# Kernel optimization log

Hardware: AMD Instinct MI355X
Metric: run time of the kernel (lower is better)

## Reference

```python
import jax, jax.numpy as jnp
import numpy as np
import math

N_HEAD = 16

def setup_inputs() -> dict:
    key = jax.random.key(0)
    ks = jax.random.split(key, 5)
    B, T, C = 4, 2048, 2048
    s = 1.0 / math.sqrt(C)
    return {
        "x": jax.random.normal(ks[0], (B, T, C), jnp.float32),
        "w_attn": jax.random.normal(ks[1], (C, 3 * C), jnp.float32) * s,
        "b_attn": jax.random.normal(ks[2], (3 * C,), jnp.float32) * 0.01,
        "w_proj": jax.random.normal(ks[3], (C, C), jnp.float32) * s,
        "b_proj": jax.random.normal(ks[4], (C,), jnp.float32) * 0.01,
    }

def reference(x, w_attn, b_attn, w_proj, b_proj):
    B, T, C = x.shape
    H = N_HEAD
    D = C // H
    # fused QKV projection: [B,T,3C] -> [3,B,H,T,D]
    qkv = (x @ w_attn + b_attn).reshape(B, T, 3, H, D).transpose(2, 0, 3, 1, 4)
    q, k, v = qkv[0], qkv[1], qkv[2]
    scale = 1.0 / math.sqrt(D)
    scores = jnp.einsum("bhqd,bhkd->bhqk", q, k) * scale  # [B,H,T,T]
    causal = jnp.tril(jnp.ones((T, T), dtype=bool))
    neg = jnp.finfo(scores.dtype).min
    scores = jnp.where(causal, scores, neg)
    attn = jax.nn.softmax(scores, axis=-1)
    y = jnp.einsum("bhqk,bhkd->bhqd", attn, v)  # [B,H,T,D]
    y = y.transpose(0, 2, 1, 3).reshape(B, T, C)
    return y @ w_proj + b_proj
```

## Files before the change

kernel.cpp:

```cpp
#include <hip/hip_runtime.h>
#include <hip/hip_bf16.h>
#include <stdint.h>

typedef unsigned short u16;
typedef __bf16 bf16x8 __attribute__((ext_vector_type(8)));
typedef unsigned short u16x8 __attribute__((ext_vector_type(8)));
typedef float f32x4 __attribute__((ext_vector_type(4)));

__device__ __forceinline__ float bf2f(u16 u){ union{float f; unsigned i;} v; v.i = ((unsigned)u)<<16; return v.f; }
__device__ __forceinline__ u16 f2bf(float f){ union{float f; unsigned i;} v; v.f=f; unsigned r = v.i + 0x7FFFu + ((v.i>>16)&1u); return (u16)(r>>16); }

__device__ __forceinline__ void async16(const void* g, void* l){
  __builtin_amdgcn_global_load_lds((const __attribute__((address_space(1))) void*)g,
                                   (__attribute__((address_space(3))) void*)l, 16, 0, 0);
}

__global__ __launch_bounds__(256) void cvt_f2b(const float* __restrict__ src, u16* __restrict__ dst, int n)
{
  int i = (blockIdx.x * 256 + threadIdx.x) * 4;
  if (i < n) {
    float4 v = *(const float4*)&src[i];
    ushort4 o;
    o.x = f2bf(v.x); o.y = f2bf(v.y); o.z = f2bf(v.z); o.w = f2bf(v.w);
    *(ushort4*)&dst[i] = o;
  }
}

__global__ __launch_bounds__(256) void transpose2d_f2b(const float* __restrict__ src, u16* __restrict__ dst,
                                                       int src_rows, int src_cols)
{
  __shared__ u16 tile[64][72];
  const int r0 = blockIdx.y << 6, c0 = blockIdx.x << 6;
  const int t = threadIdx.x;
  #pragma unroll
  for (int i=0;i<4;i++){
    int slot = t + (i<<8);
    int r = slot >> 4, cv = (slot & 15) << 2;
    float4 v = *(const float4*)&src[(size_t)(r0+r)*src_cols + c0 + cv];
    tile[r][cv+0] = f2bf(v.x); tile[r][cv+1] = f2bf(v.y);
    tile[r][cv+2] = f2bf(v.z); tile[r][cv+3] = f2bf(v.w);
  }
  __syncthreads();
  #pragma unroll
  for (int i=0;i<2;i++){
    int slot = t + (i<<8);
    int cr = slot >> 3, rv = (slot & 7) << 3;
    u16x8 v;
    #pragma unroll
    for (int e=0;e<8;e++) v[e] = tile[rv+e][cr];
    *(u16x8*)&dst[(size_t)(c0+cr)*src_rows + r0 + rv] = v;
  }
}

__global__ __launch_bounds__(256) void transpose_v(const u16* __restrict__ qkv, u16* __restrict__ vt)
{
  __shared__ u16 tile[64][72];
  const int bh = blockIdx.z;
  const int b = bh >> 4, h = bh & 15;
  const u16* src = qkv + (size_t)b*2048*6144 + 4096 + h*128;
  u16* dst = vt + (size_t)bh*128*2048;
  const int t0 = blockIdx.y << 6, d0 = blockIdx.x << 6;
  const int t = threadIdx.x;
  #pragma unroll
  for (int i=0;i<2;i++){
    int slot = t + (i<<8);
    int r = slot >> 3, cv = (slot & 7) << 3;
    *(u16x8*)&tile[r][cv] = *(const u16x8*)&src[(size_t)(t0+r)*6144 + d0 + cv];
  }
  __syncthreads();
  #pragma unroll
  for (int i=0;i<2;i++){
    int slot = t + (i<<8);
    int cr = slot >> 3, rv = (slot & 7) << 3;
    u16x8 v;
    #pragma unroll
    for (int e=0;e<8;e++) v[e] = tile[rv+e][cr];
    *(u16x8*)&dst[(size_t)(d0+cr)*2048 + t0 + rv] = v;
  }
}

template<int F32OUT>
__global__ __launch_bounds__(512, 2) void gemm8p(const u16* __restrict__ A, const u16* __restrict__ Bt,
                                                 const float* __restrict__ bias, void* __restrict__ Cv,
                                                 int M, int N, int K, int mtiles)
{
  __shared__ u16 lsA[2][2][256*32];
  __shared__ u16 lsB[2][2][256*32];
  const int tid = threadIdx.x;
  const int w = tid >> 6, lane = tid & 63;
  const int wm = w >> 2, wn = w & 3;
  const int lo = lane & 15, hi = lane >> 4;

  const int nwg = gridDim.x;
  const int bid = blockIdx.x;
  const int swz = (bid & 7) * (nwg >> 3) + (bid >> 3);
  const int mt = swz % mtiles, nt = swz / mtiles;
  const int m0 = mt << 8, n0 = nt << 8;
  const int NT = K >> 6, NI = NT >> 1;

  const int s0 = tid, s1 = tid + 512;
  const size_t off0 = (size_t)(s0>>2)*K + (size_t)((((s0&3) ^ ((s0>>3)&3))) << 3);
  const size_t off1 = (size_t)(s1>>2)*K + (size_t)((((s1&3) ^ ((s1>>3)&3))) << 3);
  const u16* Asrc = A + (size_t)m0*K;
  const u16* Bsrc = Bt + (size_t)n0*K;

  f32x4 acc[8][4];
  f32x4 z = {0.f,0.f,0.f,0.f};
  #pragma unroll
  for (int i=0;i<8;i++)
    #pragma unroll
    for (int j=0;j<4;j++) acc[i][j] = z;

  bf16x8 aE[4], aO[4], bX[4], bY[4];

#define SLOT(T, KH, AP, BP) do { \
    const u16* as_ = Asrc + (T)*64 + (KH)*32; \
    const u16* bs_ = Bsrc + (T)*64 + (KH)*32; \
    async16(as_ + off0, &(AP)[s0*8]); \
    async16(as_ + off1, &(AP)[s1*8]); \
    async16(bs_ + off0, &(BP)[s0*8]); \
    async16(bs_ + off1, &(BP)[s1*8]); \
  } while(0)

#define RDA(SET, BUF, KS, Q) do { \
    _Pragma("unroll") \
    for (int mf=0; mf<4; ++mf){ \
      int row_ = wm*128 + (Q)*64 + mf*16 + lo; \
      SET[mf] = *(const bf16x8*)&lsA[BUF][KS][row_*32 + ((hi ^ ((row_>>1) & 3)) << 3)]; \
    } } while(0)

#define RDB(SET, BUF, KS) do { \
    _Pragma("unroll") \
    for (int nf=0; nf<4; ++nf){ \
      int row_ = wn*64 + nf*16 + lo; \
      SET[nf] = *(const bf16x8*)&lsB[BUF][KS][row_*32 + ((hi ^ ((row_>>1) & 3)) << 3)]; \
    } } while(0)

#define MM(Q, AS, BS) do { \
    __builtin_amdgcn_s_setprio(1); \
    _Pragma("unroll") \
    for (int mf=0; mf<4; ++mf) \
      _Pragma("unroll") \
      for (int nf=0; nf<4; ++nf) \
        acc[(Q)*4+mf][nf] = __builtin_amdgcn_mfma_f32_16x16x32_bf16(AS[mf], BS[nf], acc[(Q)*4+mf][nf], 0,0,0); \
    __builtin_amdgcn_s_setprio(0); \
  } while(0)

#define LGK4 do { asm volatile("s_waitcnt lgkmcnt(4)" ::: "memory"); __builtin_amdgcn_sched_barrier(0); } while(0)
#define LGK8 do { asm volatile("s_waitcnt lgkmcnt(8)" ::: "memory"); __builtin_amdgcn_sched_barrier(0); } while(0)
#define LGK0 do { asm volatile("s_waitcnt lgkmcnt(0)" ::: "memory"); __builtin_amdgcn_sched_barrier(0); } while(0)
#define VM8 asm volatile("s_waitcnt vmcnt(8)" ::: "memory")
#define VM4 asm volatile("s_waitcnt vmcnt(4)" ::: "memory")
#define VM0 asm volatile("s_waitcnt vmcnt(0)" ::: "memory")
#define ENDP do { __builtin_amdgcn_s_barrier(); __builtin_amdgcn_sched_barrier(0); } while(0)

  SLOT(0, 0, lsA[0][0], lsB[0][0]);
  SLOT(0, 1, lsA[0][1], lsB[0][1]);
  SLOT(1, 0, lsA[1][0], lsB[1][0]);
  VM8;
  __builtin_amdgcn_s_barrier();
  __builtin_amdgcn_sched_barrier(0);
  RDA(aO, 0,0, 0); RDB(bX, 0,0);

  #pragma unroll 1
  for (int i = 0; i < NI-1; ++i){
    const int t0 = 2*i;
    RDA(aE, 0,0, 1); SLOT(t0+1,1, lsA[1][1], lsB[1][1]); LGK4; MM(0, aO, bX); VM8; ENDP;
    RDA(aO, 0,1, 0); RDB(bY, 0,1);                       LGK8; MM(1, aE, bX);      ENDP;
    RDA(aE, 0,1, 1); SLOT(t0+2,0, lsA[0][0], lsB[0][0]); LGK4; MM(0, aO, bY); VM8; ENDP;
    RDA(aO, 1,0, 0); RDB(bX, 1,0);                       LGK8; MM(1, aE, bY);      ENDP;
    RDA(aE, 1,0, 1); SLOT(t0+2,1, lsA[0][1], lsB[0][1]); LGK4; MM(0, aO, bX); VM8; ENDP;
    RDA(aO, 1,1, 0); RDB(bY, 1,1);                       LGK8; MM(1, aE, bX);      ENDP;
    RDA(aE, 1,1, 1); SLOT(t0+3,0, lsA[1][0], lsB[1][0]); LGK4; MM(0, aO, bY); VM8; ENDP;
    RDA(aO, 0,0, 0); RDB(bX, 0,0);                       LGK8; MM(1, aE, bY);      ENDP;
  }
  RDA(aE, 0,0, 1); SLOT(NT-1,1, lsA[1][1], lsB[1][1]);   LGK4; MM(0, aO, bX); VM8; ENDP;
  RDA(aO, 0,1, 0); RDB(bY, 0,1);                         LGK8; MM(1, aE, bX);      ENDP;
  RDA(aE, 0,1, 1);                                       LGK4; MM(0, aO, bY); VM4; ENDP;
  RDA(aO, 1,0, 0); RDB(bX, 1,0);                         LGK8; MM(1, aE, bY);      ENDP;
  RDA(aE, 1,0, 1);                                       LGK4; MM(0, aO, bX); VM0; ENDP;
  RDA(aO, 1,1, 0); RDB(bY, 1,1);                         LGK8; MM(1, aE, bX);      ENDP;
  RDA(aE, 1,1, 1);                                       LGK4; MM(0, aO, bY);      ENDP;
                                                         LGK0; MM(1, aE, bY);

#undef SLOT
#undef RDA
#undef RDB
#undef MM

  float bv[4];
  #pragma unroll
  for (int nf=0;nf<4;nf++) bv[nf] = bias[n0 + wn*64 + nf*16 + lo];
  #pragma unroll
  for (int am=0;am<8;am++){
    int row = m0 + wm*128 + am*16 + hi*4;
    #pragma unroll
    for (int nf=0;nf<4;nf++){
      int col = n0 + wn*64 + nf*16 + lo;
      #pragma unroll
      for (int r=0;r<4;r++){
        float vv = acc[am][nf][r] + bv[nf];
        if (F32OUT) ((float*)Cv)[(size_t)(row+r)*N + col] = vv;
        else        ((u16*)Cv)[(size_t)(row+r)*N + col] = f2bf(vv);
      }
    }
  }
}

__global__ __launch_bounds__(512, 4) void attn_fwd(const u16* __restrict__ qkv, const u16* __restrict__ vt,
                                                   u16* __restrict__ y)
{
  __shared__ u16 kb[2][64*128];
  __shared__ u16 vb[2][128*64];
  __shared__ u16 plds[8][16*64];
  const int bh = blockIdx.y;
  const int b = bh >> 4, h = bh & 15;
  const int pair = blockIdx.x;
  const int tid = threadIdx.x;
  const int w = tid >> 6, lane = tid & 63;
  const int lo = lane & 15, hi = lane >> 4;

  const u16* Qb = qkv + (size_t)b*2048*6144 + h*128;
  const u16* Kb = Qb + 2048;
  const u16* Vb = vt + (size_t)bh*128*2048;
  u16* pw = &plds[w][0];
  const float sc = 0.08838834764831845f * 1.4426950408889634f;
  f32x4 z = {0.f,0.f,0.f,0.f};

  #pragma unroll 1
  for (int seg = 0; seg < 2; ++seg){
    const int qt = seg ? pair : 15 - pair;
    const int qw = qt*128 + w*16;
    const int nt = qt*2 + 2;

    bf16x8 qf[4];
    #pragma unroll
    for (int kd=0;kd<4;kd++)
      qf[kd] = *(const bf16x8*)&Qb[(size_t)(qw + lo)*6144 + kd*32 + hi*8];

    f32x4 o[8];
    #pragma unroll
    for (int dj=0;dj<8;dj++) o[dj] = z;
    float mx[4], lsum[4];
    #pragma unroll
    for (int r=0;r<4;r++){ mx[r] = -3.0e38f; lsum[r] = 0.f; }

    #pragma unroll
    for (int i=0;i<2;i++){
      int slot = i*512 + tid;
      int kr = slot >> 4;
      int kc = ((slot & 15) << 4) ^ ((kr & 7) << 4);
      async16(Kb + (size_t)kr*6144 + (kc >> 1), &kb[0][(size_t)(i*512 + w*64)*8]);
      int vr = slot >> 3;
      int vc = ((slot & 7) << 4) ^ ((vr & 7) << 4);
      async16(Vb + (size_t)vr*2048 + (vc >> 1), &vb[0][(size_t)(i*512 + w*64)*8]);
    }
    __syncthreads();

    #pragma unroll 1
    for (int it = 0; it < nt; ++it){
      const int k0 = it*64;
      if (it + 1 < nt){
        const int kn = (it+1)*64;
        u16* kdst = kb[(it+1)&1];
        u16* vdst = vb[(it+1)&1];
        #pragma unroll
        for (int i=0;i<2;i++){
          int slot = i*512 + tid;
          int kr = slot >> 4;
          int kc = ((slot & 15) << 4) ^ ((kr & 7) << 4);
          async16(Kb + (size_t)(kn + kr)*6144 + (kc >> 1), &kdst[(size_t)(i*512 + w*64)*8]);
          int vr = slot >> 3;
          int vc = ((slot & 7) << 4) ^ ((vr & 7) << 4);
          async16(Vb + (size_t)vr*2048 + kn + (vc >> 1), &vdst[(size_t)(i*512 + w*64)*8]);
        }
      }
      if (k0 <= qw + 15){
        const u16* kcur = kb[it&1];
        const u16* vcur = vb[it&1];
        f32x4 s[4];
        #pragma unroll
        for (int t=0;t<4;t++) s[t] = z;
        __builtin_amdgcn_s_setprio(1);
        #pragma unroll
        for (int t=0;t<4;t++){
          #pragma unroll
          for (int kd=0;kd<4;kd++){
            int row = t*16 + lo;
            int cb = (kd*64 + hi*16) ^ ((lo & 7) << 4);
            bf16x8 kk = *(const bf16x8*)&kcur[row*128 + (cb >> 1)];
            s[t] = __builtin_amdgcn_mfma_f32_16x16x32_bf16(qf[kd], kk, s[t], 0,0,0);
          }
        }
        __builtin_amdgcn_s_setprio(0);

        if (k0 + 63 > qw) {
          #pragma unroll
          for (int t=0;t<4;t++)
            #pragma unroll
            for (int r=0;r<4;r++){
              int q = qw + hi*4 + r;
              int k = k0 + t*16 + lo;
              if (k > q) s[t][r] = -3.0e38f;
            }
        }
        #pragma unroll
        for (int r=0;r<4;r++){
          float tm = fmaxf(fmaxf(s[0][r], s[1][r]), fmaxf(s[2][r], s[3][r]));
          tm = fmaxf(tm, __shfl_xor(tm, 1));
          tm = fmaxf(tm, __shfl_xor(tm, 2));
          tm = fmaxf(tm, __shfl_xor(tm, 4));
          tm = fmaxf(tm, __shfl_xor(tm, 8));
          tm *= sc;
          float mn = fmaxf(mx[r], tm);
          float al = exp2f(mx[r] - mn);
          mx[r] = mn;
          float p0 = exp2f(fmaf(s[0][r], sc, -mn));
          float p1 = exp2f(fmaf(s[1][r], sc, -mn));
          float p2 = exp2f(fmaf(s[2][r], sc, -mn));
          float p3 = exp2f(fmaf(s[3][r], sc, -mn));
          float sum = (p0 + p1) + (p2 + p3);
          sum += __shfl_xor(sum, 1);
          sum += __shfl_xor(sum, 2);
          sum += __shfl_xor(sum, 4);
          sum += __shfl_xor(sum, 8);
          lsum[r] = lsum[r]*al + sum;
          #pragma unroll
          for (int dj=0;dj<8;dj++) o[dj][r] *= al;
          int row = hi*4 + r;
          int sw = (row & 7) << 4;
          u16* prow = pw + row*64;
          prow[((     lo*2) ^ sw) >> 1] = f2bf(p0);
          prow[((32 + lo*2) ^ sw) >> 1] = f2bf(p1);
          prow[((64 + lo*2) ^ sw) >> 1] = f2bf(p2);
          prow[((96 + lo*2) ^ sw) >> 1] = f2bf(p3);
        }

        bf16x8 pa[2];
        #pragma unroll
        for (int kf=0;kf<2;kf++)
          pa[kf] = *(const bf16x8*)&pw[(lo*128 + ((kf*64 + hi*16) ^ ((lo & 7) << 4))) >> 1];
        __builtin_amdgcn_s_setprio(1);
        #pragma unroll
        for (int dj=0;dj<8;dj++){
          int row = dj*16 + lo;
          int cb0 = (hi*16)      ^ ((lo & 7) << 4);
          int cb1 = (64 + hi*16) ^ ((lo & 7) << 4);
          bf16x8 vv0 = *(const bf16x8*)&vcur[row*64 + (cb0 >> 1)];
          bf16x8 vv1 = *(const bf16x8*)&vcur[row*64 + (cb1 >> 1)];
          o[dj] = __builtin_amdgcn_mfma_f32_16x16x32_bf16(pa[0], vv0, o[dj], 0,0,0);
          o[dj] = __builtin_amdgcn_mfma_f32_16x16x32_bf16(pa[1], vv1, o[dj], 0,0,0);
        }
        __builtin_amdgcn_s_setprio(0);
      }
      __syncthreads();
    }

    #pragma unroll
    for (int r=0;r<4;r++){
      float inv = 1.0f / lsum[r];
      size_t row = (size_t)(b*2048 + qw + hi*4 + r);
      #pragma unroll
      for (int dj=0;dj<8;dj++)
        y[row*2048 + h*128 + dj*16 + lo] = f2bf(o[dj][r] * inv);
    }
    __syncthreads();
  }
}

extern "C" void kernel_launch(void* const* d_in, const int* in_sizes, int n_in,
                              void* d_out, int out_size, void* d_ws, size_t ws_size,
                              hipStream_t stream) {
  (void)in_sizes; (void)n_in; (void)out_size; (void)ws_size;
  const float* x      = (const float*)d_in[0];
  const float* w_attn = (const float*)d_in[1];
  const float* b_attn = (const float*)d_in[2];
  const float* w_proj = (const float*)d_in[3];
  const float* b_proj = (const float*)d_in[4];
  float* out = (float*)d_out;

  char* ws = (char*)d_ws;
  u16* xbf = (u16*)(ws);
  u16* wT  = (u16*)(ws + 33554432);
  u16* pT  = (u16*)(ws + 58720256);
  u16* qkv = (u16*)(ws + 67108864);
  u16* vt  = (u16*)(ws + 167772160);
  u16* y   = xbf;

  cvt_f2b<<<16384, 256, 0, stream>>>(x, xbf, 8192*2048);
  transpose2d_f2b<<<dim3(96,32), 256, 0, stream>>>(w_attn, wT, 2048, 6144);
  transpose2d_f2b<<<dim3(32,32), 256, 0, stream>>>(w_proj, pT, 2048, 2048);
  gemm8p<0><<<768, 512, 0, stream>>>(xbf, wT, b_attn, qkv, 8192, 6144, 2048, 32);
  transpose_v<<<dim3(2,32,64), 256, 0, stream>>>(qkv, vt);
  attn_fwd<<<dim3(8,64), 512, 0, stream>>>(qkv, vt, y);
  gemm8p<1><<<256, 512, 0, stream>>>(y, pT, b_proj, out, 8192, 2048, 2048, 32);
}
```

Before: 506.9 us.

## Switch GEMM to 32x32x16 MFMA and reorder tile mapping to N-major

The GEMM kernel now uses 32x32x16 bf16 MFMA instructions instead of 16x16x32. The aim is fewer LDS fragment reads per FLOP and higher MFMA throughput per instruction. LDS read addressing and the epilogue row/column mapping are reworked to match the 32x32 accumulator layout. The tile index decomposition is also changed so that consecutive swizzled blocks walk along N instead of M, which alters L2 reuse. The epilogue now stores with 32-wide column groups, so its write coalescing pattern changes.

```diff
diff --git a/kernel.cpp b/kernel.cpp
--- a/kernel.cpp
+++ b/kernel.cpp
@@ -6,6 +6,7 @@
 typedef __bf16 bf16x8 __attribute__((ext_vector_type(8)));
 typedef unsigned short u16x8 __attribute__((ext_vector_type(8)));
 typedef float f32x4 __attribute__((ext_vector_type(4)));
+typedef float f32x16 __attribute__((ext_vector_type(16)));
 
 __device__ __forceinline__ float bf2f(u16 u){ union{float f; unsigned i;} v; v.i = ((unsigned)u)<<16; return v.f; }
 __device__ __forceinline__ u16 f2bf(float f){ union{float f; unsigned i;} v; v.f=f; unsigned r = v.i + 0x7FFFu + ((v.i>>16)&1u); return (u16)(r>>16); }
@@ -82,19 +83,19 @@
 template<int F32OUT>
 __global__ __launch_bounds__(512, 2) void gemm8p(const u16* __restrict__ A, const u16* __restrict__ Bt,
                                                  const float* __restrict__ bias, void* __restrict__ Cv,
-                                                 int M, int N, int K, int mtiles)
+                                                 int M, int N, int K, int ntn)
 {
   __shared__ u16 lsA[2][2][256*32];
   __shared__ u16 lsB[2][2][256*32];
   const int tid = threadIdx.x;
   const int w = tid >> 6, lane = tid & 63;
   const int wm = w >> 2, wn = w & 3;
-  const int lo = lane & 15, hi = lane >> 4;
+  const int l5 = lane >> 5, l31 = lane & 31;
 
   const int nwg = gridDim.x;
   const int bid = blockIdx.x;
   const int swz = (bid & 7) * (nwg >> 3) + (bid >> 3);
-  const int mt = swz % mtiles, nt = swz / mtiles;
+  const int nt = swz % ntn, mt = swz / ntn;
   const int m0 = mt << 8, n0 = nt << 8;
   const int NT = K >> 6, NI = NT >> 1;
 
@@ -104,12 +105,13 @@
   const u16* Asrc = A + (size_t)m0*K;
   const u16* Bsrc = Bt + (size_t)n0*K;
 
-  f32x4 acc[8][4];
-  f32x4 z = {0.f,0.f,0.f,0.f};
-  #pragma unroll
-  for (int i=0;i<8;i++)
-    #pragma unroll
-    for (int j=0;j<4;j++) acc[i][j] = z;
+  f32x16 acc[4][2];
+  #pragma unroll
+  for (int i=0;i<4;i++)
+    #pragma unroll
+    for (int j=0;j<2;j++)
+      #pragma unroll
+      for (int e=0;e<16;e++) acc[i][j][e] = 0.f;
 
   bf16x8 aE[4], aO[4], bX[4], bY[4];
 
@@ -124,25 +126,35 @@
 
 #define RDA(SET, BUF, KS, Q) do { \
     _Pragma("unroll") \
-    for (int mf=0; mf<4; ++mf){ \
-      int row_ = wm*128 + (Q)*64 + mf*16 + lo; \
-      SET[mf] = *(const bf16x8*)&lsA[BUF][KS][row_*32 + ((hi ^ ((row_>>1) & 3)) << 3)]; \
+    for (int mb=0; mb<2; ++mb){ \
+      int row_ = wm*128 + (Q)*64 + mb*32 + l31; \
+      _Pragma("unroll") \
+      for (int ks=0; ks<2; ++ks){ \
+        int g_ = (ks*2 + l5) ^ ((row_>>1) & 3); \
+        SET[mb*2+ks] = *(const bf16x8*)&lsA[BUF][KS][row_*32 + (g_<<3)]; \
+      } \
     } } while(0)
 
 #define RDB(SET, BUF, KS) do { \
     _Pragma("unroll") \
-    for (int nf=0; nf<4; ++nf){ \
-      int row_ = wn*64 + nf*16 + lo; \
-      SET[nf] = *(const bf16x8*)&lsB[BUF][KS][row_*32 + ((hi ^ ((row_>>1) & 3)) << 3)]; \
+    for (int nb=0; nb<2; ++nb){ \
+      int row_ = wn*64 + nb*32 + l31; \
+      _Pragma("unroll") \
+      for (int ks=0; ks<2; ++ks){ \
+        int g_ = (ks*2 + l5) ^ ((row_>>1) & 3); \
+        SET[nb*2+ks] = *(const bf16x8*)&lsB[BUF][KS][row_*32 + (g_<<3)]; \
+      } \
     } } while(0)
 
 #define MM(Q, AS, BS) do { \
     __builtin_amdgcn_s_setprio(1); \
     _Pragma("unroll") \
-    for (int mf=0; mf<4; ++mf) \
+    for (int mb=0; mb<2; ++mb) \
       _Pragma("unroll") \
-      for (int nf=0; nf<4; ++nf) \
-        acc[(Q)*4+mf][nf] = __builtin_amdgcn_mfma_f32_16x16x32_bf16(AS[mf], BS[nf], acc[(Q)*4+mf][nf], 0,0,0); \
+      for (int nb=0; nb<2; ++nb) \
+        _Pragma("unroll") \
+        for (int ks=0; ks<2; ++ks) \
+          acc[(Q)*2+mb][nb] = __builtin_amdgcn_mfma_f32_32x32x16_bf16(AS[mb*2+ks], BS[nb*2+ks], acc[(Q)*2+mb][nb], 0,0,0); \
     __builtin_amdgcn_s_setprio(0); \
   } while(0)
 
@@ -188,20 +200,20 @@
 #undef RDB
 #undef MM
 
-  float bv[4];
-  #pragma unroll
-  for (int nf=0;nf<4;nf++) bv[nf] = bias[n0 + wn*64 + nf*16 + lo];
-  #pragma unroll
-  for (int am=0;am<8;am++){
-    int row = m0 + wm*128 + am*16 + hi*4;
-    #pragma unroll
-    for (int nf=0;nf<4;nf++){
-      int col = n0 + wn*64 + nf*16 + lo;
+  float bv[2];
+  #pragma unroll
+  for (int nb=0;nb<2;nb++) bv[nb] = bias[n0 + wn*64 + nb*32 + l31];
+  #pragma unroll
+  for (int am=0;am<4;am++){
+    #pragma unroll
+    for (int nb=0;nb<2;nb++){
+      int col = n0 + wn*64 + nb*32 + l31;
       #pragma unroll
-      for (int r=0;r<4;r++){
-        float vv = acc[am][nf][r] + bv[nf];
-        if (F32OUT) ((float*)Cv)[(size_t)(row+r)*N + col] = vv;
-        else        ((u16*)Cv)[(size_t)(row+r)*N + col] = f2bf(vv);
+      for (int r=0;r<16;r++){
+        int row = m0 + wm*128 + am*32 + (r&3) + 8*(r>>2) + 4*l5;
+        float vv = acc[am][nb][r] + bv[nb];
+        if (F32OUT) ((float*)Cv)[(size_t)row*N + col] = vv;
+        else        ((u16*)Cv)[(size_t)row*N + col] = f2bf(vv);
       }
     }
   }
@@ -390,8 +402,8 @@
   cvt_f2b<<<16384, 256, 0, stream>>>(x, xbf, 8192*2048);
   transpose2d_f2b<<<dim3(96,32), 256, 0, stream>>>(w_attn, wT, 2048, 6144);
   transpose2d_f2b<<<dim3(32,32), 256, 0, stream>>>(w_proj, pT, 2048, 2048);
-  gemm8p<0><<<768, 512, 0, stream>>>(xbf, wT, b_attn, qkv, 8192, 6144, 2048, 32);
+  gemm8p<0><<<768, 512, 0, stream>>>(xbf, wT, b_attn, qkv, 8192, 6144, 2048, 24);
   transpose_v<<<dim3(2,32,64), 256, 0, stream>>>(qkv, vt);
   attn_fwd<<<dim3(8,64), 512, 0, stream>>>(qkv, vt, y);
-  gemm8p<1><<<256, 512, 0, stream>>>(y, pT, b_proj, out, 8192, 2048, 2048, 32);
-}
+  gemm8p<1><<<256, 512, 0, stream>>>(y, pT, b_proj, out, 8192, 2048, 2048, 8);
+}
```

Result: no change. 512.5 us (+1.1%).
